# Optimization experiments

Measured on AMD Instinct MI355X. Metric: run time of the kernel, lower is better.

## Reference

```python
import jax, jax.numpy as jnp
import numpy as np

L, B, V, E, H = 128, 64, 10000, 512, 512


def setup_inputs() -> dict:
    key = jax.random.key(0)
    ks = jax.random.split(key, 12)
    s = 0.05
    seq = jax.random.randint(ks[0], (L, B), 0, V, dtype=jnp.int32)
    seq_length = jnp.full((B,), L, dtype=jnp.int32)  # equal lengths -> pack/pad identity
    return {
        "seq": seq,
        "seq_length": seq_length,
        "emb": jax.random.normal(ks[1], (V, E), jnp.float32) * 0.01,  # matches init.normal std=0.01
        "W_ih_f": jax.random.normal(ks[2], (3 * H, E), jnp.float32) * s,
        "W_hh_f": jax.random.normal(ks[3], (3 * H, H), jnp.float32) * s,
        "b_ih_f": jax.random.normal(ks[4], (3 * H,), jnp.float32) * s,
        "b_hh_f": jax.random.normal(ks[5], (3 * H,), jnp.float32) * s,
        "W_ih_b": jax.random.normal(ks[6], (3 * H, E), jnp.float32) * s,
        "W_hh_b": jax.random.normal(ks[7], (3 * H, H), jnp.float32) * s,
        "b_ih_b": jax.random.normal(ks[8], (3 * H,), jnp.float32) * s,
        "b_hh_b": jax.random.normal(ks[9], (3 * H,), jnp.float32) * s,
        "dec_W": jax.random.normal(ks[10], (V, 2 * H), jnp.float32) * s,
        "dec_b": jax.random.normal(ks[11], (V,), jnp.float32) * s,
    }


def _gru(x_emb, W_ih, W_hh, b_ih, b_hh, reverse):
    # x_emb: [L, B, E]; PyTorch GRU cell equations.
    gx = jnp.einsum('lbe,ge->lbg', x_emb, W_ih) + b_ih  # [L, B, 3H]
    h0 = jnp.zeros((x_emb.shape[1], W_hh.shape[1]), x_emb.dtype)

    def step(h, gx_t):
        gh = h @ W_hh.T + b_hh
        r = jax.nn.sigmoid(gx_t[:, :H] + gh[:, :H])
        z = jax.nn.sigmoid(gx_t[:, H:2 * H] + gh[:, H:2 * H])
        n = jnp.tanh(gx_t[:, 2 * H:] + r * gh[:, 2 * H:])
        h_new = (1.0 - z) * n + z * h
        return h_new, h_new

    _, ys = jax.lax.scan(step, h0, gx, reverse=reverse)
    return ys  # [L, B, H], aligned with input positions


def reference(seq, seq_length, emb, W_ih_f, W_hh_f, b_ih_f, b_hh_f,
              W_ih_b, W_hh_b, b_ih_b, b_hh_b, dec_W, dec_b):
    x = emb[seq]  # [L, B, E]; dropout=0 (eval) -> identity
    out_f = _gru(x, W_ih_f, W_hh_f, b_ih_f, b_hh_f, reverse=False)  # [L, B, H]
    out_b = _gru(x, W_ih_b, W_hh_b, b_ih_b, b_hh_b, reverse=True)   # [L, B, H]
    # EditType.REPLACE: fwd state before the edited token, bwd state after it
    out = jnp.concatenate([out_f[0:L - 2], out_b[2:L]], axis=2)  # [L-2, B, 2H]
    logits = jnp.einsum('lbh,vh->lbv', out, dec_W) + dec_b       # [L-2, B, V]
    return jax.nn.log_softmax(logits, axis=-1)
```

## Files before the change

kernel.cpp:

```cpp
#include <hip/hip_runtime.h>
#include <hip/hip_bf16.h>
#include <stdint.h>

#define LL 128
#define BB 64
#define VV 10000
#define EE 512
#define HH 512
#define G3 1536
#define MROWS 8192
#define DM 8064
#define D2H 1024
#define NPAD 10112
#define FP 16
#define NTILE_M 63
#define NTILE_N 79

typedef __bf16 bf16x8 __attribute__((ext_vector_type(8)));
typedef float f32x4 __attribute__((ext_vector_type(4)));
typedef int i32x4 __attribute__((ext_vector_type(4)));
typedef unsigned int u32x4 __attribute__((ext_vector_type(4)));
typedef unsigned int u32x2 __attribute__((ext_vector_type(2)));
typedef unsigned short u16;
typedef unsigned long long u64;

static __device__ __forceinline__ float bf2f(u16 u) {
  unsigned int x = ((unsigned int)u) << 16;
  return __builtin_bit_cast(float, x);
}
static __device__ __forceinline__ u16 f2bf(float f) {
  unsigned int x = __builtin_bit_cast(unsigned int, f);
  unsigned int r = x + 0x7FFFu + ((x >> 16) & 1u);
  return (u16)(r >> 16);
}
static __device__ __forceinline__ signed char q8(float v) {
  float r = fminf(fmaxf(rintf(v), -127.f), 127.f);
  return (signed char)(int)r;
}

static __device__ __forceinline__ void cstore16(void* p, u32x4 v) {
  asm volatile("global_store_dwordx4 %0, %1, off sc0 sc1" :: "v"(p), "v"(v) : "memory");
}
static __device__ __forceinline__ void cstore8(void* p, u64 v) {
  u32x2 d = __builtin_bit_cast(u32x2, v);
  asm volatile("global_store_dwordx2 %0, %1, off sc0 sc1" :: "v"(p), "v"(d) : "memory");
}
static __device__ __forceinline__ void flagstore4(void* p, int v) {
  asm volatile("global_store_dword %0, %1, off sc0 sc1" :: "v"(p), "v"(v) : "memory");
}
static __device__ __forceinline__ int flagload4(const void* p) {
  int v;
  asm volatile("global_load_dword %0, %1, off sc0 sc1\n\ts_waitcnt vmcnt(0)"
               : "=v"(v) : "v"(p) : "memory");
  return v;
}
static __device__ __forceinline__ void gload_lds16(const void* g, void* s) {
  __builtin_amdgcn_global_load_lds(
      (const __attribute__((address_space(1))) unsigned int*)g,
      (__attribute__((address_space(3))) unsigned int*)s, 16, 0, 0);
}

__global__ void k_cast4(const float4* __restrict__ s0, const float4* __restrict__ s1,
                        const float4* __restrict__ s2, const float4* __restrict__ s3,
                        ushort4* __restrict__ d0, ushort4* __restrict__ d1,
                        ushort4* __restrict__ d2, ushort4* __restrict__ d3, int n4) {
  const float4* s; ushort4* d;
  switch (blockIdx.y) {
    case 0: s = s0; d = d0; break;
    case 1: s = s1; d = d1; break;
    case 2: s = s2; d = d2; break;
    default: s = s3; d = d3; break;
  }
  int i = blockIdx.x * blockDim.x + threadIdx.x;
  if (i < n4) {
    float4 v = s[i];
    ushort4 o;
    o.x = f2bf(v.x); o.y = f2bf(v.y); o.z = f2bf(v.z); o.w = f2bf(v.w);
    d[i] = o;
  }
}

__global__ __launch_bounds__(256) void k_quant_w(const float* __restrict__ W,
                                                 signed char* __restrict__ Q,
                                                 float* __restrict__ wscale) {
  const int v = blockIdx.x;
  const int tid = threadIdx.x;
  const int l = tid & 63, w = tid >> 6;
  float4 x = *(const float4*)(W + (long)v * 1024 + tid * 4);
  float m = fmaxf(fmaxf(fabsf(x.x), fabsf(x.y)), fmaxf(fabsf(x.z), fabsf(x.w)));
#pragma unroll
  for (int off = 32; off; off >>= 1) m = fmaxf(m, __shfl_xor(m, off));
  __shared__ float red[4];
  __shared__ float s_inv;
  if (l == 0) red[w] = m;
  __syncthreads();
  if (tid == 0) {
    float mm = fmaxf(fmaxf(red[0], red[1]), fmaxf(red[2], red[3]));
    mm = fmaxf(mm, 1e-12f);
    s_inv = 127.f / mm;
    wscale[v] = mm / (127.f * 127.f);
  }
  __syncthreads();
  float inv = s_inv;
  char4 o;
  o.x = q8(x.x * inv); o.y = q8(x.y * inv); o.z = q8(x.z * inv); o.w = q8(x.w * inv);
  *(char4*)(Q + (long)v * 1024 + tid * 4) = o;
}

__global__ void k_embed(const int* __restrict__ seq, const float* __restrict__ emb,
                        u16* __restrict__ x) {
  int rb = blockIdx.x;
  int v = seq[rb];
  const float4* s = (const float4*)(emb + (long)v * EE);
  ushort4* d = (ushort4*)(x + (long)rb * EE);
  int t = threadIdx.x;
  float4 val = s[t];
  ushort4 o;
  o.x = f2bf(val.x); o.y = f2bf(val.y); o.z = f2bf(val.z); o.w = f2bf(val.w);
  d[t] = o;
}

__global__ __launch_bounds__(256) void k_gemm_gx(
    const u16* __restrict__ A, const u16* __restrict__ W0, const u16* __restrict__ W1,
    const float* __restrict__ b0, const float* __restrict__ b1, u16* __restrict__ C)
{
  __shared__ char smem[32768];
  const int tid = threadIdx.x;
  const int l = tid & 63;
  const int w = tid >> 6;
  const int wr = w >> 1, wc = w & 1;
  const long tM = (long)blockIdx.x * 128;
  const long tN = (long)blockIdx.y * 128;
  const int z = blockIdx.z;
  const u16* B = z ? W1 : W0;
  const float* bias = z ? b1 : b0;
  u16* Cz = C + (size_t)z * MROWS * G3;

  f32x4 acc[4][4];
#pragma unroll
  for (int m = 0; m < 4; m++)
#pragma unroll
    for (int n = 0; n < 4; n++) acc[m][n] = {0.f, 0.f, 0.f, 0.f};

  for (int kt = 0; kt < 8; ++kt) {
    const int k0 = kt << 6;
#pragma unroll
    for (int i = 0; i < 4; i++) {
      int cchunk = w * 4 + i;
      int c = cchunk * 64 + l;
      int row = c >> 3, k8 = c & 7;
      gload_lds16(A + (tM + row) * EE + k0 + k8 * 8, smem + cchunk * 1024);
      gload_lds16(B + (tN + row) * EE + k0 + k8 * 8, smem + 16384 + cchunk * 1024);
    }
    __syncthreads();
#pragma unroll
    for (int kk = 0; kk < 2; kk++) {
      const int kb = kk * 64 + ((l >> 4) * 16);
      bf16x8 af[4], bfr[4];
#pragma unroll
      for (int m = 0; m < 4; m++) {
        int ra = wr * 64 + m * 16 + (l & 15);
        af[m] = *(const bf16x8*)(smem + ra * 128 + kb);
      }
#pragma unroll
      for (int n = 0; n < 4; n++) {
        int rb2 = wc * 64 + n * 16 + (l & 15);
        bfr[n] = *(const bf16x8*)(smem + 16384 + rb2 * 128 + kb);
      }
#pragma unroll
      for (int m = 0; m < 4; m++)
#pragma unroll
        for (int n = 0; n < 4; n++)
          acc[m][n] = __builtin_amdgcn_mfma_f32_16x16x32_bf16(af[m], bfr[n], acc[m][n], 0, 0, 0);
    }
    __syncthreads();
  }
#pragma unroll
  for (int n = 0; n < 4; n++) {
    long col = tN + wc * 64 + n * 16 + (l & 15);
    float bv = bias[col];
#pragma unroll
    for (int m = 0; m < 4; m++) {
      long row = tM + wr * 64 + m * 16 + ((l >> 4) * 4);
#pragma unroll
      for (int r = 0; r < 4; r++)
        Cz[(row + r) * G3 + col] = f2bf(acc[m][n][r] + bv);
    }
  }
}


static __device__ void gru_body(
    int blk, int dir, int tid, char* lds,
    const u16* __restrict__ Whh_all,
    const float* __restrict__ bhh_f, const float* __restrict__ bhh_b,
    const u16* __restrict__ gx_all, u16* __restrict__ hsteps,
    signed char* __restrict__ catq, int* __restrict__ bar16)
{
  const int l = tid & 63, w = tid >> 6;
  const u16* Whh = Whh_all + (long)dir * G3 * HH;
  const float* bhh = dir ? bhh_b : bhh_f;
  const u16* gx = gx_all + (long)dir * MROWS * G3;

  char* Wl = lds;
  u16 (*hstage)[32] = (u16(*)[32])(lds + 96 * 1024);
  signed char (*hstageq)[32] = (signed char(*)[32])(lds + 96 * 1024 + 4096);

  for (int c = tid; c < 6144; c += 256) {
    int lr = c >> 6;
    int k8 = c & 63;
    int gr = (lr >> 5) * HH + blk * 32 + (lr & 31);
    uint4 v = *(const uint4*)(Whh + (long)gr * HH + k8 * 8);
    *(uint4*)(Wl + lr * 1024 + ((k8 * 16) ^ ((lr & 7) << 4))) = v;
  }
  float bh[6];
#pragma unroll
  for (int n = 0; n < 6; n++) {
    int c = n * 16 + (l & 15);
    bh[n] = bhh[(c >> 5) * HH + blk * 32 + (c & 31)];
  }
  float hreg[4][2] = {};
  __syncthreads();

  const int lrow = w * 16 + ((l >> 4) * 4);
  const int srow = tid >> 2, schunk = tid & 3;

  u16 gxn[3][4][2];
  {
    const int lpos0 = dir ? (LL - 1) : 0;
#pragma unroll
    for (int r = 0; r < 4; r++) {
      const u16* gxr = gx + ((long)lpos0 * BB + (lrow + r)) * G3 + blk * 32;
#pragma unroll
      for (int g = 0; g < 3; g++)
#pragma unroll
        for (int p = 0; p < 2; p++)
          gxn[g][r][p] = gxr[g * HH + p * 16 + (l & 15)];
    }
  }

  for (int t = 0; t < LL; ++t) {
    const int lpos = dir ? (LL - 1 - t) : t;
    const u16* hsrc = hsteps + ((size_t)t * 2 + dir) * BB * HH;

    u16 gxv[3][4][2];
#pragma unroll
    for (int g = 0; g < 3; g++)
#pragma unroll
      for (int r = 0; r < 4; r++)
#pragma unroll
        for (int p = 0; p < 2; p++) gxv[g][r][p] = gxn[g][r][p];

    bf16x8 af[16];
    {
      const u16* hrow = hsrc + (w * 16 + (l & 15)) * HH + ((l >> 4) * 8);
#pragma unroll
      for (int kc = 0; kc < 16; kc++) af[kc] = *(const bf16x8*)(hrow + kc * 32);
    }

    f32x4 acc[6];
#pragma unroll
    for (int n = 0; n < 6; n++) acc[n] = {0.f, 0.f, 0.f, 0.f};
#pragma unroll
    for (int kc = 0; kc < 16; kc++) {
      const int kb = kc * 64 + ((l >> 4) * 16);
#pragma unroll
      for (int n = 0; n < 6; n++) {
        int lr = n * 16 + (l & 15);
        bf16x8 bfr = *(const bf16x8*)(Wl + lr * 1024 + (kb ^ ((l & 7) << 4)));
        acc[n] = __builtin_amdgcn_mfma_f32_16x16x32_bf16(af[kc], bfr, acc[n], 0, 0, 0);
      }
    }

#pragma unroll
    for (int r = 0; r < 4; r++) {
#pragma unroll
      for (int p = 0; p < 2; p++) {
        float ghr = acc[0 + p][r] + bh[0 + p];
        float ghz = acc[2 + p][r] + bh[2 + p];
        float ghn = acc[4 + p][r] + bh[4 + p];
        float xr = bf2f(gxv[0][r][p]);
        float xz = bf2f(gxv[1][r][p]);
        float xn = bf2f(gxv[2][r][p]);
        float ar = fminf(fmaxf(xr + ghr, -30.f), 30.f);
        float az = fminf(fmaxf(xz + ghz, -30.f), 30.f);
        float rg = 1.f / (1.f + __expf(-ar));
        float zg = 1.f / (1.f + __expf(-az));
        float an = fminf(fmaxf(xn + rg * ghn, -30.f), 30.f);
        float e2 = __expf(-2.f * an);
        float ng = (1.f - e2) / (1.f + e2);
        float hn = (1.f - zg) * ng + zg * hreg[r][p];
        hreg[r][p] = hn;
        hstage[lrow + r][p * 16 + (l & 15)] = f2bf(hn);
        hstageq[lrow + r][p * 16 + (l & 15)] = q8(hn * 127.f);
      }
    }
    __syncthreads();

    u32x4 hv = *(const u32x4*)&hstage[srow][schunk * 8];
    u64 hq = *(const u64*)&hstageq[srow][schunk * 8];
    if (t < LL - 1)
      cstore16(hsteps + ((size_t)(t + 1) * 2 + dir) * BB * HH + srow * HH + blk * 32 + schunk * 8, hv);
    if (dir == 0) {
      if (lpos < LL - 2)
        cstore8(catq + ((long)lpos * BB + srow) * D2H + blk * 32 + schunk * 8, hq);
    } else {
      if (lpos >= 2)
        cstore8(catq + ((long)(lpos - 2) * BB + srow) * D2H + HH + blk * 32 + schunk * 8, hq);
    }
    if (t < LL - 1) {
      asm volatile("s_waitcnt vmcnt(0)" ::: "memory");
      __syncthreads();
      if (tid == 0)
        flagstore4(&bar16[((dir * LL + t) * 16 + blk) * FP], 1);
      {
        const int lposn = dir ? (LL - 2 - t) : (t + 1);
#pragma unroll
        for (int r = 0; r < 4; r++) {
          const u16* gxr = gx + ((long)lposn * BB + (lrow + r)) * G3 + blk * 32;
#pragma unroll
          for (int g = 0; g < 3; g++)
#pragma unroll
            for (int p = 0; p < 2; p++)
              gxn[g][r][p] = gxr[g * HH + p * 16 + (l & 15)];
        }
      }
      const int* flg = bar16 + (dir * LL + t) * 16 * FP;
      for (;;) {
        int v = 1;
        if (l < 16) v = flagload4(&flg[l * FP]);
        if (__all(v != 0)) break;
      }
      __builtin_amdgcn_sched_barrier(0);
    }
  }
}

static __device__ void dec_body(
    int tid, char* smem, int* tk_sh,
    const signed char* __restrict__ A, const signed char* __restrict__ B,
    const float* __restrict__ wscale, const float* __restrict__ bias,
    void* __restrict__ Cv, int outbf,
    int* __restrict__ ticket, const int* __restrict__ bar16)
{
  const int l = tid & 63;
  const int w = tid >> 6;
  const int wr = w >> 1, wc = w & 1;

  for (;;) {
    if (tid == 0)
      *tk_sh = __hip_atomic_fetch_add(ticket, 1, __ATOMIC_RELAXED, __HIP_MEMORY_SCOPE_AGENT);
    __syncthreads();
    const int n = *tk_sh;
    __syncthreads();
    if (n >= NTILE_M * NTILE_N) return;
    const int k = n / NTILE_N, j = n % NTILE_N;
    const int mi = (k & 1) ? (31 + ((k + 1) >> 1)) : (31 - (k >> 1));
    const long tM = (long)mi * 128;
    const long tN = (long)j * 128;

    {
      const int tf = 2 * mi + 1;
      const int tb = 125 - 2 * mi;
      const int* fp = (l < 16)
          ? bar16 + ((0 * LL + tf) * 16 + l) * FP
          : bar16 + ((1 * LL + tb) * 16 + (l & 15)) * FP;
      for (;;) {
        int v = 1;
        if (l < 32) v = flagload4(fp);
        if (__all(v != 0)) break;
      }
    }

    i32x4 acc[4][4];
#pragma unroll
    for (int m = 0; m < 4; m++)
#pragma unroll
      for (int nn = 0; nn < 4; nn++) acc[m][nn] = {0, 0, 0, 0};

    for (int kt = 0; kt < 8; ++kt) {
      const int k0 = kt << 7;
#pragma unroll
      for (int i = 0; i < 4; i++) {
        int jj = w * 4 + i;
        int row = jj * 8 + (l >> 3);
        int k16 = l & 7;
        gload_lds16(A + (tM + row) * 1024 + k0 + k16 * 16, smem + jj * 1024);
        gload_lds16(B + (tN + row) * 1024 + k0 + k16 * 16, smem + 16384 + jj * 1024);
      }
      __syncthreads();
#pragma unroll
      for (int ks = 0; ks < 2; ks++) {
        const int kb = ks * 64 + ((l >> 4) * 16);
        i32x4 af[4], bfr[4];
#pragma unroll
        for (int m = 0; m < 4; m++) {
          int ra = wr * 64 + m * 16 + (l & 15);
          af[m] = *(const i32x4*)(smem + ra * 128 + kb);
        }
#pragma unroll
        for (int nn = 0; nn < 4; nn++) {
          int rb2 = wc * 64 + nn * 16 + (l & 15);
          bfr[nn] = *(const i32x4*)(smem + 16384 + rb2 * 128 + kb);
        }
#pragma unroll
        for (int m = 0; m < 4; m++)
#pragma unroll
          for (int nn = 0; nn < 4; nn++)
            acc[m][nn] = __builtin_amdgcn_mfma_i32_16x16x64_i8(af[m], bfr[nn], acc[m][nn], 0, 0, 0);
      }
      __syncthreads();
    }
#pragma unroll
    for (int nn = 0; nn < 4; nn++) {
      long col = tN + wc * 64 + nn * 16 + (l & 15);
      if (col < VV) {
        float sc = wscale[col];
        float bv = bias[col];
#pragma unroll
        for (int m = 0; m < 4; m++) {
          long row = tM + wr * 64 + m * 16 + ((l >> 4) * 4);
#pragma unroll
          for (int r = 0; r < 4; r++) {
            float vv = (float)acc[m][nn][r] * sc + bv;
            if (outbf) ((u16*)Cv)[(row + r) * NPAD + col] = f2bf(vv);
            else       ((float*)Cv)[(row + r) * VV + col] = vv;
          }
        }
      }
    }
  }
}

__global__ __launch_bounds__(256) void k_fused(
    const u16* __restrict__ Whh_all,
    const float* __restrict__ bhh_f, const float* __restrict__ bhh_b,
    const u16* __restrict__ gx_all, u16* __restrict__ hsteps,
    signed char* __restrict__ catq, int* __restrict__ bar16,
    const signed char* __restrict__ decWq, const float* __restrict__ wscale,
    const float* __restrict__ decb, void* __restrict__ Cv, int outbf,
    int* __restrict__ ticket)
{
  __shared__ __align__(16) char lds[104448];
  __shared__ int tk_sh;
  const int bid = blockIdx.x;
  const int tid = threadIdx.x;
  if (bid < 32) {
    gru_body(bid >> 1, bid & 1, tid, lds, Whh_all, bhh_f, bhh_b, gx_all,
             hsteps, catq, bar16);
  } else {
    dec_body(tid, lds, &tk_sh, catq, decWq, wscale, decb, Cv, outbf, ticket, bar16);
  }
}

__global__ __launch_bounds__(256) void k_lsm(float* __restrict__ out) {
  const long row = blockIdx.x;
  float* p = out + row * VV;
  const int tid = threadIdx.x;
  const int l = tid & 63, w = tid >> 6;
  __shared__ float red[8];

  float4 v[10];
  float m = -1e30f;
#pragma unroll
  for (int j = 0; j < 10; j++) {
    int idx = j * 256 + tid;
    if (idx < 2500) {
      v[j] = *(float4*)(p + idx * 4);
      m = fmaxf(m, fmaxf(fmaxf(v[j].x, v[j].y), fmaxf(v[j].z, v[j].w)));
    }
  }
#pragma unroll
  for (int off = 32; off; off >>= 1) m = fmaxf(m, __shfl_xor(m, off));
  if (l == 0) red[w] = m;
  __syncthreads();
  m = fmaxf(fmaxf(red[0], red[1]), fmaxf(red[2], red[3]));

  float s = 0.f;
#pragma unroll
  for (int j = 0; j < 10; j++) {
    int idx = j * 256 + tid;
    if (idx < 2500) {
      s += __expf(v[j].x - m) + __expf(v[j].y - m) + __expf(v[j].z - m) + __expf(v[j].w - m);
    }
  }
#pragma unroll
  for (int off = 32; off; off >>= 1) s += __shfl_xor(s, off);
  if (l == 0) red[4 + w] = s;
  __syncthreads();
  s = red[4] + red[5] + red[6] + red[7];
  float lse = m + logf(s);

#pragma unroll
  for (int j = 0; j < 10; j++) {
    int idx = j * 256 + tid;
    if (idx < 2500) {
      float4 o;
      o.x = v[j].x - lse; o.y = v[j].y - lse; o.z = v[j].z - lse; o.w = v[j].w - lse;
      *(float4*)(p + idx * 4) = o;
    }
  }
}

__global__ __launch_bounds__(256) void k_lsm_b(const u16* __restrict__ lg,
                                               float* __restrict__ out) {
  const long row = blockIdx.x;
  const u16* p = lg + row * NPAD;
  float* q = out + row * VV;
  const int tid = threadIdx.x;
  const int l = tid & 63, w = tid >> 6;
  __shared__ float red[8];

  float v[5][8];
  float m = -1e30f;
#pragma unroll
  for (int j = 0; j < 5; j++) {
    int idx8 = j * 256 + tid;
    if (idx8 < 1250) {
      u32x4 u = *(const u32x4*)(p + idx8 * 8);
#pragma unroll
      for (int e = 0; e < 4; e++) {
        v[j][2 * e]     = bf2f((u16)(u[e] & 0xffffu));
        v[j][2 * e + 1] = bf2f((u16)(u[e] >> 16));
      }
#pragma unroll
      for (int e = 0; e < 8; e++) m = fmaxf(m, v[j][e]);
    }
  }
#pragma unroll
  for (int off = 32; off; off >>= 1) m = fmaxf(m, __shfl_xor(m, off));
  if (l == 0) red[w] = m;
  __syncthreads();
  m = fmaxf(fmaxf(red[0], red[1]), fmaxf(red[2], red[3]));

  float s = 0.f;
#pragma unroll
  for (int j = 0; j < 5; j++) {
    int idx8 = j * 256 + tid;
    if (idx8 < 1250) {
#pragma unroll
      for (int e = 0; e < 8; e++) s += __expf(v[j][e] - m);
    }
  }
#pragma unroll
  for (int off = 32; off; off >>= 1) s += __shfl_xor(s, off);
  if (l == 0) red[4 + w] = s;
  __syncthreads();
  s = red[4] + red[5] + red[6] + red[7];
  float lse = m + logf(s);

#pragma unroll
  for (int j = 0; j < 5; j++) {
    int idx8 = j * 256 + tid;
    if (idx8 < 1250) {
      float4 a, b;
      a.x = v[j][0] - lse; a.y = v[j][1] - lse; a.z = v[j][2] - lse; a.w = v[j][3] - lse;
      b.x = v[j][4] - lse; b.y = v[j][5] - lse; b.z = v[j][6] - lse; b.w = v[j][7] - lse;
      *(float4*)(q + idx8 * 8) = a;
      *(float4*)(q + idx8 * 8 + 4) = b;
    }
  }
}

extern "C" void kernel_launch(void* const* d_in, const int* in_sizes, int n_in,
                              void* d_out, int out_size, void* d_ws, size_t ws_size,
                              hipStream_t stream) {
  const int*   seq  = (const int*)d_in[0];
  const float* emb  = (const float*)d_in[2];
  const float* Wihf = (const float*)d_in[3];
  const float* Whhf = (const float*)d_in[4];
  const float* bihf = (const float*)d_in[5];
  const float* bhhf = (const float*)d_in[6];
  const float* Wihb = (const float*)d_in[7];
  const float* Whhb = (const float*)d_in[8];
  const float* bihb = (const float*)d_in[9];
  const float* bhhb = (const float*)d_in[10];
  const float* decW = (const float*)d_in[11];
  const float* decb = (const float*)d_in[12];

  char* ws = (char*)d_ws;
  size_t off = 0;
  u16* Whh_bf = (u16*)(ws + off); off += (size_t)2 * G3 * HH * 2;
  u16* Wih_bf = (u16*)(ws + off); off += (size_t)2 * G3 * EE * 2;
  signed char* decWq = (signed char*)(ws + off); off += (size_t)NPAD * 1024;
  float* wscale = (float*)(ws + off); off += (size_t)NPAD * 4;
  u16* xb = (u16*)(ws + off); off += (size_t)MROWS * EE * 2;
  u16* gxb = (u16*)(ws + off); off += (size_t)2 * MROWS * G3 * 2;
  signed char* catq = (signed char*)(ws + off); off += (size_t)DM * D2H;
  u16* hsteps = (u16*)(ws + off); off += (size_t)(LL + 1) * 2 * BB * HH * 2;
  int* bar16 = (int*)(ws + off); off += (size_t)2 * LL * 16 * FP * 4;
  int* ticket = (int*)(ws + off); off += 64;
  u16* logitsb = (u16*)(ws + off);
  const size_t logits_bytes = (size_t)DM * NPAD * 2;
  const bool use_bf16_logits = (ws_size >= off + logits_bytes);

  (void)hipMemsetAsync(hsteps, 0, (size_t)2 * BB * HH * 2, stream);
  (void)hipMemsetAsync(bar16, 0, (size_t)2 * LL * 16 * FP * 4 + 64, stream);

  const int n4w = G3 * HH / 4;
  k_cast4<<<dim3((n4w + 255) / 256, 4), 256, 0, stream>>>(
      (const float4*)Whhf, (const float4*)Whhb, (const float4*)Wihf, (const float4*)Wihb,
      (ushort4*)Whh_bf, (ushort4*)(Whh_bf + G3 * HH),
      (ushort4*)Wih_bf, (ushort4*)(Wih_bf + G3 * EE), n4w);
  k_quant_w<<<VV, 256, 0, stream>>>(decW, decWq, wscale);
  k_embed<<<MROWS, 128, 0, stream>>>(seq, emb, xb);

  k_gemm_gx<<<dim3(64, 12, 2), 256, 0, stream>>>(xb, Wih_bf, Wih_bf + G3 * EE,
                                                 bihf, bihb, gxb);

  void* Cv = use_bf16_logits ? (void*)logitsb : (void*)d_out;
  k_fused<<<dim3(256), 256, 0, stream>>>(Whh_bf, bhhf, bhhb, gxb, hsteps, catq,
                                         bar16, decWq, wscale, decb, Cv,
                                         use_bf16_logits ? 1 : 0, ticket);

  if (use_bf16_logits) k_lsm_b<<<DM, 256, 0, stream>>>(logitsb, (float*)d_out);
  else                 k_lsm<<<DM, 256, 0, stream>>>((float*)d_out);
}
```

Before: 982.2 us.

## Merge prep kernels into one and fold log-softmax into fused persistent kernel

Combines the weight cast, decoder-weight quantization and embedding kernels into a single k_prep launch. It also moves the bf16 log-softmax pass into the persistent k_fused kernel. Decoder blocks signal completion through a counter, and every block then pulls rows from a ticket queue once all 224 decoder blocks are done. This is meant to remove launch gaps and kernel tails, at the cost of a global spin-wait and a hard dependence on all 256 blocks being co-resident.

New measurement: 1.090 ms. +11.0%, slower.

```diff
diff --git a/kernel.cpp b/kernel.cpp
--- a/kernel.cpp
+++ b/kernel.cpp
@@ -15,6 +15,8 @@
 #define FP 16
 #define NTILE_M 63
 #define NTILE_N 79
+#define DECQ (NTILE_M * NTILE_N)
+#define DECB 224
 
 typedef __bf16 bf16x8 __attribute__((ext_vector_type(8)));
 typedef float f32x4 __attribute__((ext_vector_type(4)));
@@ -60,64 +62,64 @@
       (__attribute__((address_space(3))) unsigned int*)s, 16, 0, 0);
 }
 
-__global__ void k_cast4(const float4* __restrict__ s0, const float4* __restrict__ s1,
-                        const float4* __restrict__ s2, const float4* __restrict__ s3,
-                        ushort4* __restrict__ d0, ushort4* __restrict__ d1,
-                        ushort4* __restrict__ d2, ushort4* __restrict__ d3, int n4) {
-  const float4* s; ushort4* d;
-  switch (blockIdx.y) {
-    case 0: s = s0; d = d0; break;
-    case 1: s = s1; d = d1; break;
-    case 2: s = s2; d = d2; break;
-    default: s = s3; d = d3; break;
-  }
-  int i = blockIdx.x * blockDim.x + threadIdx.x;
-  if (i < n4) {
+__global__ __launch_bounds__(256) void k_prep(
+    const float* __restrict__ decW, signed char* __restrict__ decWq,
+    float* __restrict__ wscale,
+    const int* __restrict__ seq, const float* __restrict__ emb,
+    u16* __restrict__ xb,
+    const float* __restrict__ Whhf, const float* __restrict__ Whhb,
+    const float* __restrict__ Wihf, const float* __restrict__ Wihb,
+    u16* __restrict__ Whh_bf, u16* __restrict__ Wih_bf)
+{
+  __shared__ float red[4];
+  __shared__ float s_inv;
+  const int bid = blockIdx.x;
+  const int tid = threadIdx.x;
+
+  if (bid < VV) {
+    const int v = bid;
+    const int l = tid & 63, w = tid >> 6;
+    float4 x = *(const float4*)(decW + (long)v * 1024 + tid * 4);
+    float m = fmaxf(fmaxf(fabsf(x.x), fabsf(x.y)), fmaxf(fabsf(x.z), fabsf(x.w)));
+#pragma unroll
+    for (int off = 32; off; off >>= 1) m = fmaxf(m, __shfl_xor(m, off));
+    if (l == 0) red[w] = m;
+    __syncthreads();
+    if (tid == 0) {
+      float mm = fmaxf(fmaxf(red[0], red[1]), fmaxf(red[2], red[3]));
+      mm = fmaxf(mm, 1e-12f);
+      s_inv = 127.f / mm;
+      wscale[v] = mm / (127.f * 127.f);
+    }
+    __syncthreads();
+    float inv = s_inv;
+    char4 o;
+    o.x = q8(x.x * inv); o.y = q8(x.y * inv); o.z = q8(x.z * inv); o.w = q8(x.w * inv);
+    *(char4*)(decWq + (long)v * 1024 + tid * 4) = o;
+  } else if (bid < VV + 4096) {
+    int rb = (bid - VV) * 2 + (tid >> 7);
+    int t = tid & 127;
+    int v = seq[rb];
+    float4 val = ((const float4*)(emb + (long)v * EE))[t];
+    ushort4 o;
+    o.x = f2bf(val.x); o.y = f2bf(val.y); o.z = f2bf(val.z); o.w = f2bf(val.w);
+    ((ushort4*)(xb + (long)rb * EE))[t] = o;
+  } else {
+    int c = bid - VV - 4096;
+    int tensor = c / 768;
+    int i = (c % 768) * 256 + tid;
+    const float4* s; ushort4* d;
+    switch (tensor) {
+      case 0: s = (const float4*)Whhf; d = (ushort4*)Whh_bf; break;
+      case 1: s = (const float4*)Whhb; d = (ushort4*)(Whh_bf + G3 * HH); break;
+      case 2: s = (const float4*)Wihf; d = (ushort4*)Wih_bf; break;
+      default: s = (const float4*)Wihb; d = (ushort4*)(Wih_bf + G3 * EE); break;
+    }
     float4 v = s[i];
     ushort4 o;
     o.x = f2bf(v.x); o.y = f2bf(v.y); o.z = f2bf(v.z); o.w = f2bf(v.w);
     d[i] = o;
   }
-}
-
-__global__ __launch_bounds__(256) void k_quant_w(const float* __restrict__ W,
-                                                 signed char* __restrict__ Q,
-                                                 float* __restrict__ wscale) {
-  const int v = blockIdx.x;
-  const int tid = threadIdx.x;
-  const int l = tid & 63, w = tid >> 6;
-  float4 x = *(const float4*)(W + (long)v * 1024 + tid * 4);
-  float m = fmaxf(fmaxf(fabsf(x.x), fabsf(x.y)), fmaxf(fabsf(x.z), fabsf(x.w)));
-#pragma unroll
-  for (int off = 32; off; off >>= 1) m = fmaxf(m, __shfl_xor(m, off));
-  __shared__ float red[4];
-  __shared__ float s_inv;
-  if (l == 0) red[w] = m;
-  __syncthreads();
-  if (tid == 0) {
-    float mm = fmaxf(fmaxf(red[0], red[1]), fmaxf(red[2], red[3]));
-    mm = fmaxf(mm, 1e-12f);
-    s_inv = 127.f / mm;
-    wscale[v] = mm / (127.f * 127.f);
-  }
-  __syncthreads();
-  float inv = s_inv;
-  char4 o;
-  o.x = q8(x.x * inv); o.y = q8(x.y * inv); o.z = q8(x.z * inv); o.w = q8(x.w * inv);
-  *(char4*)(Q + (long)v * 1024 + tid * 4) = o;
-}
-
-__global__ void k_embed(const int* __restrict__ seq, const float* __restrict__ emb,
-                        u16* __restrict__ x) {
-  int rb = blockIdx.x;
-  int v = seq[rb];
-  const float4* s = (const float4*)(emb + (long)v * EE);
-  ushort4* d = (ushort4*)(x + (long)rb * EE);
-  int t = threadIdx.x;
-  float4 val = s[t];
-  ushort4 o;
-  o.x = f2bf(val.x); o.y = f2bf(val.y); o.z = f2bf(val.z); o.w = f2bf(val.w);
-  d[t] = o;
 }
 
 __global__ __launch_bounds__(256) void k_gemm_gx(
@@ -341,7 +343,8 @@
     const signed char* __restrict__ A, const signed char* __restrict__ B,
     const float* __restrict__ wscale, const float* __restrict__ bias,
     void* __restrict__ Cv, int outbf,
-    int* __restrict__ ticket, const int* __restrict__ bar16)
+    int* __restrict__ ticket, const int* __restrict__ bar16,
+    int* __restrict__ blocks_done)
 {
   const int l = tid & 63;
   const int w = tid >> 6;
@@ -353,7 +356,13 @@
     __syncthreads();
     const int n = *tk_sh;
     __syncthreads();
-    if (n >= NTILE_M * NTILE_N) return;
+    if (n >= DECQ) {
+      asm volatile("s_waitcnt vmcnt(0)" ::: "memory");
+      __syncthreads();
+      if (tid == 0)
+        __hip_atomic_fetch_add(blocks_done, 1, __ATOMIC_RELEASE, __HIP_MEMORY_SCOPE_AGENT);
+      return;
+    }
     const int k = n / NTILE_N, j = n % NTILE_N;
     const int mi = (k & 1) ? (31 + ((k + 1) >> 1)) : (31 - (k >> 1));
     const long tM = (long)mi * 128;
@@ -429,6 +438,85 @@
         }
       }
     }
+    __syncthreads();
+  }
+}
+
+static __device__ void lsm_phase(
+    int tid, char* lds, int* tk_sh,
+    const u16* __restrict__ lg, float* __restrict__ out,
+    int* __restrict__ ticket_lsm, int* __restrict__ blocks_done)
+{
+  if (tid == 0) {
+    while (__hip_atomic_load(blocks_done, __ATOMIC_ACQUIRE, __HIP_MEMORY_SCOPE_AGENT) < DECB)
+      __builtin_amdgcn_s_sleep(8);
+  }
+  __syncthreads();
+
+  float* red = (float*)lds;
+  const int l = tid & 63, w = tid >> 6;
+  for (;;) {
+    if (tid == 0)
+      *tk_sh = __hip_atomic_fetch_add(ticket_lsm, 1, __ATOMIC_RELAXED, __HIP_MEMORY_SCOPE_AGENT);
+    __syncthreads();
+    const int n = *tk_sh;
+    __syncthreads();
+    if (n >= DM) return;
+
+    const long row = n;
+    const u16* p = lg + row * NPAD;
+    float* q = out + row * VV;
+
+    float v[5][8];
+    float m = -1e30f;
+#pragma unroll
+    for (int j = 0; j < 5; j++) {
+      int idx8 = j * 256 + tid;
+      if (idx8 < 1250) {
+        u32x4 u = *(const u32x4*)(p + idx8 * 8);
+#pragma unroll
+        for (int e = 0; e < 4; e++) {
+          v[j][2 * e]     = bf2f((u16)(u[e] & 0xffffu));
+          v[j][2 * e + 1] = bf2f((u16)(u[e] >> 16));
+        }
+#pragma unroll
+        for (int e = 0; e < 8; e++) m = fmaxf(m, v[j][e]);
+      }
+    }
+#pragma unroll
+    for (int off = 32; off; off >>= 1) m = fmaxf(m, __shfl_xor(m, off));
+    if (l == 0) red[w] = m;
+    __syncthreads();
+    m = fmaxf(fmaxf(red[0], red[1]), fmaxf(red[2], red[3]));
+
+    float s = 0.f;
+#pragma unroll
+    for (int j = 0; j < 5; j++) {
+      int idx8 = j * 256 + tid;
+      if (idx8 < 1250) {
+#pragma unroll
+        for (int e = 0; e < 8; e++) s += __expf(v[j][e] - m);
+      }
+    }
+#pragma unroll
+    for (int off = 32; off; off >>= 1) s += __shfl_xor(s, off);
+    if (l == 0) red[4 + w] = s;
+    __syncthreads();
+    s = red[4] + red[5] + red[6] + red[7];
+    float lse = m + logf(s);
+
+#pragma unroll
+    for (int j = 0; j < 5; j++) {
+      int idx8 = j * 256 + tid;
+      if (idx8 < 1250) {
+        float4 a, b;
+        a.x = v[j][0] - lse; a.y = v[j][1] - lse; a.z = v[j][2] - lse; a.w = v[j][3] - lse;
+        b.x = v[j][4] - lse; b.y = v[j][5] - lse; b.z = v[j][6] - lse; b.w = v[j][7] - lse;
+        *(float4*)(q + idx8 * 8) = a;
+        *(float4*)(q + idx8 * 8 + 4) = b;
+      }
+    }
+    __syncthreads();
   }
 }
 
@@ -439,7 +527,7 @@
     signed char* __restrict__ catq, int* __restrict__ bar16,
     const signed char* __restrict__ decWq, const float* __restrict__ wscale,
     const float* __restrict__ decb, void* __restrict__ Cv, int outbf,
-    int* __restrict__ ticket)
+    int* __restrict__ ticket, float* __restrict__ dout)
 {
   __shared__ __align__(16) char lds[104448];
   __shared__ int tk_sh;
@@ -449,8 +537,11 @@
     gru_body(bid >> 1, bid & 1, tid, lds, Whh_all, bhh_f, bhh_b, gx_all,
              hsteps, catq, bar16);
   } else {
-    dec_body(tid, lds, &tk_sh, catq, decWq, wscale, decb, Cv, outbf, ticket, bar16);
-  }
+    dec_body(tid, lds, &tk_sh, catq, decWq, wscale, decb, Cv, outbf,
+             ticket, bar16, ticket + 24);
+  }
+  if (outbf)
+    lsm_phase(tid, lds, &tk_sh, (const u16*)Cv, dout, ticket + 16, ticket + 24);
 }
 
 __global__ __launch_bounds__(256) void k_lsm(float* __restrict__ out) {
@@ -498,66 +589,6 @@
       float4 o;
       o.x = v[j].x - lse; o.y = v[j].y - lse; o.z = v[j].z - lse; o.w = v[j].w - lse;
       *(float4*)(p + idx * 4) = o;
-    }
-  }
-}
-
-__global__ __launch_bounds__(256) void k_lsm_b(const u16* __restrict__ lg,
-                                               float* __restrict__ out) {
-  const long row = blockIdx.x;
-  const u16* p = lg + row * NPAD;
-  float* q = out + row * VV;
-  const int tid = threadIdx.x;
-  const int l = tid & 63, w = tid >> 6;
-  __shared__ float red[8];
-
-  float v[5][8];
-  float m = -1e30f;
-#pragma unroll
-  for (int j = 0; j < 5; j++) {
-    int idx8 = j * 256 + tid;
-    if (idx8 < 1250) {
-      u32x4 u = *(const u32x4*)(p + idx8 * 8);
-#pragma unroll
-      for (int e = 0; e < 4; e++) {
-        v[j][2 * e]     = bf2f((u16)(u[e] & 0xffffu));
-        v[j][2 * e + 1] = bf2f((u16)(u[e] >> 16));
-      }
-#pragma unroll
-      for (int e = 0; e < 8; e++) m = fmaxf(m, v[j][e]);
-    }
-  }
-#pragma unroll
-  for (int off = 32; off; off >>= 1) m = fmaxf(m, __shfl_xor(m, off));
-  if (l == 0) red[w] = m;
-  __syncthreads();
-  m = fmaxf(fmaxf(red[0], red[1]), fmaxf(red[2], red[3]));
-
-  float s = 0.f;
-#pragma unroll
-  for (int j = 0; j < 5; j++) {
-    int idx8 = j * 256 + tid;
-    if (idx8 < 1250) {
-#pragma unroll
-      for (int e = 0; e < 8; e++) s += __expf(v[j][e] - m);
-    }
-  }
-#pragma unroll
-  for (int off = 32; off; off >>= 1) s += __shfl_xor(s, off);
-  if (l == 0) red[4 + w] = s;
-  __syncthreads();
-  s = red[4] + red[5] + red[6] + red[7];
-  float lse = m + logf(s);
-
-#pragma unroll
-  for (int j = 0; j < 5; j++) {
-    int idx8 = j * 256 + tid;
-    if (idx8 < 1250) {
-      float4 a, b;
-      a.x = v[j][0] - lse; a.y = v[j][1] - lse; a.z = v[j][2] - lse; a.w = v[j][3] - lse;
-      b.x = v[j][4] - lse; b.y = v[j][5] - lse; b.z = v[j][6] - lse; b.w = v[j][7] - lse;
-      *(float4*)(q + idx8 * 8) = a;
-      *(float4*)(q + idx8 * 8 + 4) = b;
     }
   }
 }
@@ -589,21 +620,17 @@
   signed char* catq = (signed char*)(ws + off); off += (size_t)DM * D2H;
   u16* hsteps = (u16*)(ws + off); off += (size_t)(LL + 1) * 2 * BB * HH * 2;
   int* bar16 = (int*)(ws + off); off += (size_t)2 * LL * 16 * FP * 4;
-  int* ticket = (int*)(ws + off); off += 64;
+  int* ticket = (int*)(ws + off); off += 32 * 4;
   u16* logitsb = (u16*)(ws + off);
   const size_t logits_bytes = (size_t)DM * NPAD * 2;
   const bool use_bf16_logits = (ws_size >= off + logits_bytes);
 
   (void)hipMemsetAsync(hsteps, 0, (size_t)2 * BB * HH * 2, stream);
-  (void)hipMemsetAsync(bar16, 0, (size_t)2 * LL * 16 * FP * 4 + 64, stream);
-
-  const int n4w = G3 * HH / 4;
-  k_cast4<<<dim3((n4w + 255) / 256, 4), 256, 0, stream>>>(
-      (const float4*)Whhf, (const float4*)Whhb, (const float4*)Wihf, (const float4*)Wihb,
-      (ushort4*)Whh_bf, (ushort4*)(Whh_bf + G3 * HH),
-      (ushort4*)Wih_bf, (ushort4*)(Wih_bf + G3 * EE), n4w);
-  k_quant_w<<<VV, 256, 0, stream>>>(decW, decWq, wscale);
-  k_embed<<<MROWS, 128, 0, stream>>>(seq, emb, xb);
+  (void)hipMemsetAsync(bar16, 0, (size_t)2 * LL * 16 * FP * 4 + 32 * 4, stream);
+
+  k_prep<<<dim3(VV + 4096 + 3072), 256, 0, stream>>>(
+      decW, decWq, wscale, seq, emb, xb,
+      Whhf, Whhb, Wihf, Wihb, Whh_bf, Wih_bf);
 
   k_gemm_gx<<<dim3(64, 12, 2), 256, 0, stream>>>(xb, Wih_bf, Wih_bf + G3 * EE,
                                                  bihf, bihb, gxb);
@@ -611,8 +638,8 @@
   void* Cv = use_bf16_logits ? (void*)logitsb : (void*)d_out;
   k_fused<<<dim3(256), 256, 0, stream>>>(Whh_bf, bhhf, bhhb, gxb, hsteps, catq,
                                          bar16, decWq, wscale, decb, Cv,
-                                         use_bf16_logits ? 1 : 0, ticket);
-
-  if (use_bf16_logits) k_lsm_b<<<DM, 256, 0, stream>>>(logitsb, (float*)d_out);
-  else                 k_lsm<<<DM, 256, 0, stream>>>((float*)d_out);
-}
+                                         use_bf16_logits ? 1 : 0, ticket,
+                                         (float*)d_out);
+
+  if (!use_bf16_logits) k_lsm<<<DM, 256, 0, stream>>>((float*)d_out);
+}
```
